# Performance work log

Measured on AMD Instinct MI355X. Metric: run time of the kernel, lower is better.

## Reference

```python
import jax, jax.numpy as jnp
import numpy as np

B, HW, E, H, L, T = 256, 196, 1024, 1024, 128, 48
FC_OUT = L + H + 2  # label | topic | temp | stop


def _linear_params(k, out_d, in_d):
    k1, k2 = jax.random.split(k)
    bound = 1.0 / np.sqrt(in_d)
    W = jax.random.uniform(k1, (out_d, in_d), jnp.float32, -bound, bound)
    b = jax.random.uniform(k2, (out_d,), jnp.float32, -bound, bound)
    return W, b


def setup_inputs() -> dict:
    key = jax.random.key(0)
    ks = jax.random.split(key, 8)
    image = jax.random.normal(ks[0], (B, HW, E), jnp.float32)
    label = jax.random.uniform(ks[1], (B, T, L), jnp.float32)
    # lengths sorted descending (the torch module uses @length_sorted)
    length = jnp.sort(jax.random.randint(ks[2], (B,), 1, T + 1))[::-1]
    W_h, b_h = _linear_params(ks[3], H, E)
    W_m, b_m = _linear_params(ks[4], H, E)
    W_ih, b_ih = _linear_params(ks[5], 4 * H, E + L)
    W_hh, b_hh = _linear_params(ks[6], 4 * H, H)
    W_fc, b_fc = _linear_params(ks[7], FC_OUT, H)
    return {"image": image, "label": label, "length": length,
            "W_h": W_h, "b_h": b_h, "W_m": W_m, "b_m": b_m,
            "W_ih": W_ih, "W_hh": W_hh, "b_ih": b_ih, "b_hh": b_hh,
            "W_fc": W_fc, "b_fc": b_fc}


def reference(image, label, length, W_h, b_h, W_m, b_m, W_ih, W_hh, b_ih, b_hh, W_fc, b_fc):
    # dropout is identity (eval mode)
    img_mean = image.mean(axis=1)                       # (B, E)
    h0 = jnp.tanh(img_mean @ W_h.T + b_h)               # (B, H)
    m0 = jnp.tanh(img_mean @ W_m.T + b_m)               # (B, H)
    lab_t_major = jnp.transpose(label, (1, 0, 2))       # (T, B, L)
    ts = jnp.arange(T)

    def step(carry, inp):
        h, m = carry
        lab_t, t = inp
        x = jnp.concatenate([img_mean, lab_t], axis=-1)          # (B, E+L)
        gates = x @ W_ih.T + b_ih + h @ W_hh.T + b_hh            # (B, 4H), torch order i,f,g,o
        i, f, g, o = jnp.split(gates, 4, axis=-1)
        m = jax.nn.sigmoid(f) * m + jax.nn.sigmoid(i) * jnp.tanh(g)
        h = jax.nn.sigmoid(o) * jnp.tanh(m)
        out = jax.nn.relu(h @ W_fc.T + b_fc)                     # (B, L+H+2)
        _label = out[:, :L]
        _topic = out[:, L:L + H]
        _temp = jnp.exp(out[:, L + H:L + H + 1])
        _stop = jax.nn.sigmoid(out[:, L + H + 1:])
        mask = (t < length)[:, None].astype(out.dtype)           # pad_sequence zero-padding
        return (h, m), (_label * mask, _topic * mask, _temp * mask, _stop * mask)

    _, (lab_o, top_o, temp_o, stop_o) = jax.lax.scan(step, (h0, m0), (lab_t_major, ts))
    # scan stacks on time axis -> (T, B, D); return batch-major (B, T, D)
    return tuple(jnp.transpose(a, (1, 0, 2)) for a in (lab_o, top_o, temp_o, stop_o))
```

## Files before the change

kernel.cpp:

```cpp
#include <hip/hip_runtime.h>

typedef float f32x4 __attribute__((ext_vector_type(4)));
typedef short s16x8 __attribute__((ext_vector_type(8)));
typedef unsigned short u16;

#define B_    256
#define HW_   196
#define E_    1024
#define H_    1024
#define L_    128
#define T_    48
#define FCOUT 1154
#define FCPAD 1216

#define GJOBS 128
#define FJOBS 76

__device__ __forceinline__ u16 f2bf(float x) {
  union { float f; unsigned u; } v; v.f = x;
  unsigned r = v.u + 0x7FFF + ((v.u >> 16) & 1);
  return (u16)(r >> 16);
}
__device__ __forceinline__ float sigm(float x) { return 1.f / (1.f + expf(-x)); }

__global__ __launch_bounds__(256) void cvt_bf16_v4(
    const float* __restrict__ in, u16* __restrict__ out,
    int src_rows, int in_ld, int in_off, int cols4, long total4) {
  long idx = (long)blockIdx.x * 256 + threadIdx.x;
  if (idx >= total4) return;
  int r  = (int)(idx / cols4);
  int c4 = (int)(idx % cols4) * 4;
  f32x4 v = {0.f, 0.f, 0.f, 0.f};
  if (r < src_rows) v = *(const f32x4*)&in[(size_t)r * in_ld + in_off + c4];
  ushort4 o;
  ((u16*)&o)[0] = f2bf(v[0]); ((u16*)&o)[1] = f2bf(v[1]);
  ((u16*)&o)[2] = f2bf(v[2]); ((u16*)&o)[3] = f2bf(v[3]);
  *(ushort4*)&out[idx * 4] = o;
}

__global__ __launch_bounds__(256) void img_mean_k(
    const float* __restrict__ image, u16* __restrict__ meanB) {
  int idx = blockIdx.x * 256 + threadIdx.x;
  int b  = idx >> 8;
  int e4 = (idx & 255) * 4;
  const float* p = image + (size_t)b * HW_ * E_ + e4;
  f32x4 s = {0.f, 0.f, 0.f, 0.f};
  #pragma unroll 4
  for (int hw = 0; hw < HW_; ++hw) s += *(const f32x4*)&p[(size_t)hw * E_];
  ushort4 o;
  #pragma unroll
  for (int c = 0; c < 4; ++c) ((u16*)&o)[c] = f2bf(s[c] * (1.0f / HW_));
  *(ushort4*)&meanB[(size_t)b * E_ + e4] = o;
}

template <int MODE>
__global__ __launch_bounds__(256) void gemm_nt(
    const u16* __restrict__ A, int lda, const u16* __restrict__ Bp, int ldb, int K,
    const float* __restrict__ bias1, const float* __restrict__ bias2,
    float* __restrict__ outF, u16* __restrict__ outB, int ldc) {
  __shared__ __align__(16) u16 As[64][72];
  __shared__ __align__(16) u16 Bs[64][72];

  const int m0 = blockIdx.x * 64;
  const int n0 = blockIdx.y * 64;
  const int tid  = threadIdx.x;
  const int lane = tid & 63;
  const int wave = tid >> 6;
  const int wm = wave & 1, wn = wave >> 1;
  const int quad = lane >> 4, l16 = lane & 15;
  const int loadRow = tid >> 3;
  const int loadCol = (tid & 7) * 8;

  f32x4 acc[2][2] = {};

  for (int kb = 0; kb < K; kb += 64) {
    __syncthreads();
    #pragma unroll
    for (int p = 0; p < 2; ++p) {
      int r = loadRow + p * 32;
      *(uint4*)&As[r][loadCol] = *(const uint4*)&A [(size_t)(m0 + r) * lda + kb + loadCol];
      *(uint4*)&Bs[r][loadCol] = *(const uint4*)&Bp[(size_t)(n0 + r) * ldb + kb + loadCol];
    }
    __syncthreads();
    #pragma unroll
    for (int ks = 0; ks < 64; ks += 32) {
      s16x8 a0v = *(const s16x8*)&As[wm * 32      + l16][ks + quad * 8];
      s16x8 a1v = *(const s16x8*)&As[wm * 32 + 16 + l16][ks + quad * 8];
      s16x8 b0v = *(const s16x8*)&Bs[wn * 32      + l16][ks + quad * 8];
      s16x8 b1v = *(const s16x8*)&Bs[wn * 32 + 16 + l16][ks + quad * 8];
      acc[0][0] = __builtin_amdgcn_mfma_f32_16x16x32_bf16(a0v, b0v, acc[0][0], 0, 0, 0);
      acc[0][1] = __builtin_amdgcn_mfma_f32_16x16x32_bf16(a0v, b1v, acc[0][1], 0, 0, 0);
      acc[1][0] = __builtin_amdgcn_mfma_f32_16x16x32_bf16(a1v, b0v, acc[1][0], 0, 0, 0);
      acc[1][1] = __builtin_amdgcn_mfma_f32_16x16x32_bf16(a1v, b1v, acc[1][1], 0, 0, 0);
    }
  }

  #pragma unroll
  for (int mi = 0; mi < 2; ++mi) {
    #pragma unroll
    for (int ni = 0; ni < 2; ++ni) {
      #pragma unroll
      for (int r = 0; r < 4; ++r) {
        int m = m0 + wm * 32 + mi * 16 + quad * 4 + r;
        int n = n0 + wn * 32 + ni * 16 + l16;
        float v = acc[mi][ni][r];
        if constexpr (MODE == 0) {
          outF[(size_t)m * ldc + n] = v + bias1[n] + bias2[n];
        } else if constexpr (MODE == 1) {
          outB[(size_t)m * ldc + n] = f2bf(tanhf(v + bias1[n]));
        } else {
          outF[(size_t)m * ldc + n] = tanhf(v + bias1[n]);
        }
      }
    }
  }
}

struct GS8 { u16 A[2][32][72]; u16 B[2][256][72]; };
struct FS8 { u16 A[2][64][72]; u16 B[2][64][72]; };
union __align__(16) SharedU {
  GS8 g;
  FS8 f;
  float gs[2][4][32][68];
  float fs[64][68];
};

__global__ __launch_bounds__(512) void step_k(
    const u16* __restrict__ labB,
    const u16* __restrict__ WihL,
    const u16* __restrict__ WhhB,
    const u16* __restrict__ WfcB,
    const float* __restrict__ gbase,
    const float* __restrict__ b_fc,
    const u16* __restrict__ hcur, u16* __restrict__ hnext,
    float* __restrict__ mS,
    const int* __restrict__ length,
    float* __restrict__ out,
    int p) {
  __shared__ SharedU sh;

  const int bid  = blockIdx.x;
  const int tid  = threadIdx.x;
  const int g2   = tid >> 8;
  const int gtid = tid & 255;
  const int lane = tid & 63;
  const int wave = tid >> 6;
  const int sw   = wave & 3;
  const int quad = lane >> 4, l16 = lane & 15;
  const int ar = gtid >> 3;
  const int ac = (gtid & 7) * 8;

  if (p < T_ && bid < GJOBS) {
    const int mb = bid >> 4;
    const int jb = bid & 15;
    f32x4 acc[2][4] = {};

    for (int kb = 0; kb < 9; ++kb) {
      const int seg1 = (g2 == 1) || (kb >= 2);
      const int k0 = g2 ? (448 + kb * 64) : (seg1 ? (kb - 2) * 64 : kb * 64);

      __syncthreads();
      {
        const u16* Ap = seg1
            ? hcur + (size_t)(mb * 32 + ar) * H_ + k0 + ac
            : labB + (size_t)(mb * 32 + ar) * (T_ * L_) + (size_t)p * L_ + k0 + ac;
        *(uint4*)&sh.g.A[g2][ar][ac] = *(const uint4*)Ap;
        const u16* Bw  = seg1 ? WhhB : WihL;
        const int  ldb = seg1 ? H_ : L_;
        #pragma unroll
        for (int q = 0; q < 8; ++q) {
          int rr = ar + q * 32;
          int grow = (rr >> 6) * H_ + jb * 64 + (rr & 63);
          *(uint4*)&sh.g.B[g2][rr][ac] =
              *(const uint4*)&Bw[(size_t)grow * ldb + k0 + ac];
        }
      }
      __syncthreads();
      #pragma unroll
      for (int ks = 0; ks < 64; ks += 32) {
        s16x8 av[2], bv[4];
        av[0] = *(const s16x8*)&sh.g.A[g2][l16][ks + quad * 8];
        av[1] = *(const s16x8*)&sh.g.A[g2][16 + l16][ks + quad * 8];
        #pragma unroll
        for (int ni = 0; ni < 4; ++ni)
          bv[ni] = *(const s16x8*)&sh.g.B[g2][sw * 64 + ni * 16 + l16][ks + quad * 8];
        #pragma unroll
        for (int mi = 0; mi < 2; ++mi)
          #pragma unroll
          for (int ni = 0; ni < 4; ++ni)
            acc[mi][ni] = __builtin_amdgcn_mfma_f32_16x16x32_bf16(
                av[mi], bv[ni], acc[mi][ni], 0, 0, 0);
      }
    }

    __syncthreads();
    #pragma unroll
    for (int mi = 0; mi < 2; ++mi)
      #pragma unroll
      for (int ni = 0; ni < 4; ++ni)
        #pragma unroll
        for (int r = 0; r < 4; ++r)
          sh.gs[g2][sw][mi * 16 + quad * 4 + r][ni * 16 + l16] = acc[mi][ni][r];
    __syncthreads();

    {
      const int bl = tid >> 4, j4 = (tid & 15) * 4;
      const int b = mb * 32 + bl, j = jb * 64 + j4;
      const float* gb = gbase + (size_t)b * (4 * H_) + j;
      f32x4 gi = *(const f32x4*)&sh.gs[0][0][bl][j4] + *(const f32x4*)&sh.gs[1][0][bl][j4];
      f32x4 gf = *(const f32x4*)&sh.gs[0][1][bl][j4] + *(const f32x4*)&sh.gs[1][1][bl][j4];
      f32x4 gg = *(const f32x4*)&sh.gs[0][2][bl][j4] + *(const f32x4*)&sh.gs[1][2][bl][j4];
      f32x4 go = *(const f32x4*)&sh.gs[0][3][bl][j4] + *(const f32x4*)&sh.gs[1][3][bl][j4];
      f32x4 bi  = *(const f32x4*)(gb);
      f32x4 bff = *(const f32x4*)(gb + H_);
      f32x4 bg  = *(const f32x4*)(gb + 2 * H_);
      f32x4 bo  = *(const f32x4*)(gb + 3 * H_);
      float* mp = mS + (size_t)b * H_ + j;
      f32x4 m = *(f32x4*)mp;
      ushort4 hb;
      #pragma unroll
      for (int c = 0; c < 4; ++c) {
        float I = sigm(gi[c] + bi[c]);
        float F = sigm(gf[c] + bff[c]);
        float G = tanhf(gg[c] + bg[c]);
        float O = sigm(go[c] + bo[c]);
        float mm = F * m[c] + I * G;
        m[c] = mm;
        ((u16*)&hb)[c] = f2bf(O * tanhf(mm));
      }
      *(f32x4*)mp = m;
      *(ushort4*)&hnext[(size_t)b * H_ + j] = hb;
    }
  } else if (p >= 1 && bid >= GJOBS && bid < GJOBS + FJOBS) {
    const int t   = p - 1;
    const int fid = bid - GJOBS;
    const int m0 = (fid / 19) * 64;
    const int n0 = (fid % 19) * 64;
    const int wm = sw & 1, wn = sw >> 1;
    f32x4 acc[2][2] = {};

    for (int kb = 0; kb < 8; ++kb) {
      const int k0 = g2 * 512 + kb * 64;
      __syncthreads();
      #pragma unroll
      for (int pp = 0; pp < 2; ++pp) {
        int r = ar + pp * 32;
        *(uint4*)&sh.f.A[g2][r][ac] = *(const uint4*)&hcur[(size_t)(m0 + r) * H_ + k0 + ac];
        *(uint4*)&sh.f.B[g2][r][ac] = *(const uint4*)&WfcB[(size_t)(n0 + r) * H_ + k0 + ac];
      }
      __syncthreads();
      #pragma unroll
      for (int ks = 0; ks < 64; ks += 32) {
        s16x8 a0v = *(const s16x8*)&sh.f.A[g2][wm * 32      + l16][ks + quad * 8];
        s16x8 a1v = *(const s16x8*)&sh.f.A[g2][wm * 32 + 16 + l16][ks + quad * 8];
        s16x8 b0v = *(const s16x8*)&sh.f.B[g2][wn * 32      + l16][ks + quad * 8];
        s16x8 b1v = *(const s16x8*)&sh.f.B[g2][wn * 32 + 16 + l16][ks + quad * 8];
        acc[0][0] = __builtin_amdgcn_mfma_f32_16x16x32_bf16(a0v, b0v, acc[0][0], 0, 0, 0);
        acc[0][1] = __builtin_amdgcn_mfma_f32_16x16x32_bf16(a0v, b1v, acc[0][1], 0, 0, 0);
        acc[1][0] = __builtin_amdgcn_mfma_f32_16x16x32_bf16(a1v, b0v, acc[1][0], 0, 0, 0);
        acc[1][1] = __builtin_amdgcn_mfma_f32_16x16x32_bf16(a1v, b1v, acc[1][1], 0, 0, 0);
      }
    }

    __syncthreads();
    if (g2 == 1) {
      #pragma unroll
      for (int mi = 0; mi < 2; ++mi)
        #pragma unroll
        for (int ni = 0; ni < 2; ++ni)
          #pragma unroll
          for (int r = 0; r < 4; ++r)
            sh.fs[wm * 32 + mi * 16 + quad * 4 + r][wn * 32 + ni * 16 + l16] =
                acc[mi][ni][r];
    }
    __syncthreads();
    if (g2 == 0) {
      #pragma unroll
      for (int mi = 0; mi < 2; ++mi) {
        #pragma unroll
        for (int ni = 0; ni < 2; ++ni) {
          #pragma unroll
          for (int r = 0; r < 4; ++r) {
            int ml = wm * 32 + mi * 16 + quad * 4 + r;
            int nl = wn * 32 + ni * 16 + l16;
            int m = m0 + ml;
            int n = n0 + nl;
            if (n < FCOUT) {
              float rv = fmaxf(acc[mi][ni][r] + sh.fs[ml][nl] + b_fc[n], 0.f);
              float msk = (t < length[m]) ? 1.f : 0.f;
              if (n < L_) {
                out[(size_t)m * (T_ * L_) + t * L_ + n] = rv * msk;
              } else if (n < L_ + H_) {
                out[(size_t)(B_ * T_ * L_) + (size_t)m * (T_ * H_) + t * H_ + (n - L_)] = rv * msk;
              } else if (n == L_ + H_) {
                out[(size_t)B_ * T_ * (L_ + H_) + m * T_ + t] = expf(rv) * msk;
              } else {
                out[(size_t)B_ * T_ * (L_ + H_ + 1) + m * T_ + t] = sigm(rv) * msk;
              }
            }
          }
        }
      }
    }
  }
}

extern "C" void kernel_launch(void* const* d_in, const int* in_sizes, int n_in,
                              void* d_out, int out_size, void* d_ws, size_t ws_size,
                              hipStream_t stream) {
  const float* image  = (const float*)d_in[0];
  const float* label  = (const float*)d_in[1];
  const int*   length = (const int*)  d_in[2];
  const float* W_h    = (const float*)d_in[3];
  const float* b_h    = (const float*)d_in[4];
  const float* W_m    = (const float*)d_in[5];
  const float* b_m    = (const float*)d_in[6];
  const float* W_ih   = (const float*)d_in[7];
  const float* W_hh   = (const float*)d_in[8];
  const float* b_ih   = (const float*)d_in[9];
  const float* b_hh   = (const float*)d_in[10];
  const float* W_fc   = (const float*)d_in[11];
  const float* b_fc   = (const float*)d_in[12];
  float* out = (float*)d_out;

  char* ws = (char*)d_ws;
  size_t off = 0;
  auto alloc = [&](size_t bytes) -> void* {
    void* p = ws + off;
    off = (off + bytes + 255) & ~(size_t)255;
    return p;
  };
  u16*   meanB = (u16*)  alloc((size_t)B_ * E_ * 2);
  u16*   WhB   = (u16*)  alloc((size_t)H_ * E_ * 2);
  u16*   WmB   = (u16*)  alloc((size_t)H_ * E_ * 2);
  u16*   WihE  = (u16*)  alloc((size_t)4 * H_ * E_ * 2);
  u16*   WihL  = (u16*)  alloc((size_t)4 * H_ * L_ * 2);
  u16*   WhhB  = (u16*)  alloc((size_t)4 * H_ * H_ * 2);
  u16*   WfcB  = (u16*)  alloc((size_t)FCPAD * H_ * 2);
  u16*   labB  = (u16*)  alloc((size_t)B_ * T_ * L_ * 2);
  float* gbase = (float*)alloc((size_t)B_ * 4 * H_ * 4);
  u16*   hbuf0 = (u16*)  alloc((size_t)B_ * H_ * 2);
  u16*   hbuf1 = (u16*)  alloc((size_t)B_ * H_ * 2);
  float* mS    = (float*)alloc((size_t)B_ * H_ * 4);

  auto cvt = [&](const float* in, u16* o, int rows, int src_rows, int in_ld,
                 int in_off, int cols) {
    long total4 = (long)rows * cols / 4;
    int blocks = (int)((total4 + 255) / 256);
    cvt_bf16_v4<<<blocks, 256, 0, stream>>>(in, o, src_rows, in_ld, in_off,
                                            cols / 4, total4);
  };

  cvt(W_h,  WhB,  H_,     H_,     E_,      0,  E_);
  cvt(W_m,  WmB,  H_,     H_,     E_,      0,  E_);
  cvt(W_ih, WihE, 4 * H_, 4 * H_, E_ + L_, 0,  E_);
  cvt(W_ih, WihL, 4 * H_, 4 * H_, E_ + L_, E_, L_);
  cvt(W_hh, WhhB, 4 * H_, 4 * H_, H_,      0,  H_);
  cvt(W_fc, WfcB, FCPAD,  FCOUT,  H_,      0,  H_);
  cvt(label, labB, B_, B_, T_ * L_, 0, T_ * L_);

  img_mean_k<<<(B_ * E_ / 4) / 256, 256, 0, stream>>>(image, meanB);

  gemm_nt<1><<<dim3(B_ / 64, H_ / 64), 256, 0, stream>>>(
      meanB, E_, WhB, E_, E_, b_h, nullptr, nullptr, hbuf0, H_);
  gemm_nt<2><<<dim3(B_ / 64, H_ / 64), 256, 0, stream>>>(
      meanB, E_, WmB, E_, E_, b_m, nullptr, mS, nullptr, H_);
  gemm_nt<0><<<dim3(B_ / 64, (4 * H_) / 64), 256, 0, stream>>>(
      meanB, E_, WihE, E_, E_, b_ih, b_hh, gbase, nullptr, 4 * H_);

  for (int p = 0; p <= T_; ++p) {
    u16* hcur  = (p & 1) ? hbuf1 : hbuf0;
    u16* hnext = (p & 1) ? hbuf0 : hbuf1;
    step_k<<<GJOBS + FJOBS, 512, 0, stream>>>(
        labB, WihL, WhhB, WfcB, gbase, b_fc, hcur, hnext, mS, length, out, p);
  }
}
```

Measured before the change: 1.298 ms.

## Enlarge LSTM gate tiles to 64 rows and remap block-to-tile assignment

Each gate block now covers 64 batch rows instead of 32, so the gate GEMM uses 64 blocks instead of 128. Each block reuses its loaded W_hh/W_ih tile across twice as many rows, roughly halving weight traffic per step. The two K-halves are reduced through shared memory in two phases instead of being kept as separate buffers. FC blocks are remapped onto 96 slots (76 active) with an ordering that appears to group work for cache locality. The trade-off is fewer blocks, which lowers parallelism and occupancy, and higher register pressure from the 4x4 accumulator array.

```diff
diff --git a/kernel.cpp b/kernel.cpp
--- a/kernel.cpp
+++ b/kernel.cpp
@@ -13,8 +13,9 @@
 #define FCOUT 1154
 #define FCPAD 1216
 
-#define GJOBS 128
-#define FJOBS 76
+#define GB_    64
+#define FBASE_ 64
+#define FSLOT_ 96
 
 __device__ __forceinline__ u16 f2bf(float x) {
   union { float f; unsigned u; } v; v.f = x;
@@ -116,12 +117,12 @@
   }
 }
 
-struct GS8 { u16 A[2][32][72]; u16 B[2][256][72]; };
-struct FS8 { u16 A[2][64][72]; u16 B[2][64][72]; };
+struct GS { u16 A[2][64][72]; u16 B[2][256][72]; };
+struct FS { u16 A[2][64][72]; u16 B[2][64][72]; };
 union __align__(16) SharedU {
-  GS8 g;
-  FS8 f;
-  float gs[2][4][32][68];
+  GS g;
+  FS f;
+  float ex[4][64][68];
   float fs[64][68];
 };
 
@@ -150,10 +151,11 @@
   const int ar = gtid >> 3;
   const int ac = (gtid & 7) * 8;
 
-  if (p < T_ && bid < GJOBS) {
-    const int mb = bid >> 4;
-    const int jb = bid & 15;
-    f32x4 acc[2][4] = {};
+  if (p < T_ && bid < GB_) {
+    const int q8 = bid >> 3;
+    const int mb = q8 & 3;
+    const int jb = (bid & 7) + 8 * (q8 >> 2);
+    f32x4 acc[4][4] = {};
 
     for (int kb = 0; kb < 9; ++kb) {
       const int seg1 = (g2 == 1) || (kb >= 2);
@@ -161,15 +163,19 @@
 
       __syncthreads();
       {
-        const u16* Ap = seg1
-            ? hcur + (size_t)(mb * 32 + ar) * H_ + k0 + ac
-            : labB + (size_t)(mb * 32 + ar) * (T_ * L_) + (size_t)p * L_ + k0 + ac;
-        *(uint4*)&sh.g.A[g2][ar][ac] = *(const uint4*)Ap;
+        #pragma unroll
+        for (int pp = 0; pp < 2; ++pp) {
+          int r = ar + pp * 32;
+          const u16* Ap = seg1
+              ? hcur + (size_t)(mb * 64 + r) * H_ + k0 + ac
+              : labB + (size_t)(mb * 64 + r) * (T_ * L_) + (size_t)p * L_ + k0 + ac;
+          *(uint4*)&sh.g.A[g2][r][ac] = *(const uint4*)Ap;
+        }
         const u16* Bw  = seg1 ? WhhB : WihL;
         const int  ldb = seg1 ? H_ : L_;
         #pragma unroll
-        for (int q = 0; q < 8; ++q) {
-          int rr = ar + q * 32;
+        for (int qq = 0; qq < 8; ++qq) {
+          int rr = ar + qq * 32;
           int grow = (rr >> 6) * H_ + jb * 64 + (rr & 63);
           *(uint4*)&sh.g.B[g2][rr][ac] =
               *(const uint4*)&Bw[(size_t)grow * ldb + k0 + ac];
@@ -178,14 +184,15 @@
       __syncthreads();
       #pragma unroll
       for (int ks = 0; ks < 64; ks += 32) {
-        s16x8 av[2], bv[4];
-        av[0] = *(const s16x8*)&sh.g.A[g2][l16][ks + quad * 8];
-        av[1] = *(const s16x8*)&sh.g.A[g2][16 + l16][ks + quad * 8];
+        s16x8 av[4], bv[4];
+        #pragma unroll
+        for (int mi = 0; mi < 4; ++mi)
+          av[mi] = *(const s16x8*)&sh.g.A[g2][mi * 16 + l16][ks + quad * 8];
         #pragma unroll
         for (int ni = 0; ni < 4; ++ni)
           bv[ni] = *(const s16x8*)&sh.g.B[g2][sw * 64 + ni * 16 + l16][ks + quad * 8];
         #pragma unroll
-        for (int mi = 0; mi < 2; ++mi)
+        for (int mi = 0; mi < 4; ++mi)
           #pragma unroll
           for (int ni = 0; ni < 4; ++ni)
             acc[mi][ni] = __builtin_amdgcn_mfma_f32_16x16x32_bf16(
@@ -194,48 +201,68 @@
     }
 
     __syncthreads();
-    #pragma unroll
-    for (int mi = 0; mi < 2; ++mi)
-      #pragma unroll
-      for (int ni = 0; ni < 4; ++ni)
-        #pragma unroll
-        for (int r = 0; r < 4; ++r)
-          sh.gs[g2][sw][mi * 16 + quad * 4 + r][ni * 16 + l16] = acc[mi][ni][r];
+    if (g2 == 1) {
+      #pragma unroll
+      for (int mi = 0; mi < 4; ++mi)
+        #pragma unroll
+        for (int ni = 0; ni < 4; ++ni)
+          #pragma unroll
+          for (int r = 0; r < 4; ++r)
+            sh.ex[sw][mi * 16 + quad * 4 + r][ni * 16 + l16] = acc[mi][ni][r];
+    }
+    __syncthreads();
+    if (g2 == 0) {
+      #pragma unroll
+      for (int mi = 0; mi < 4; ++mi)
+        #pragma unroll
+        for (int ni = 0; ni < 4; ++ni)
+          #pragma unroll
+          for (int r = 0; r < 4; ++r)
+            sh.ex[sw][mi * 16 + quad * 4 + r][ni * 16 + l16] += acc[mi][ni][r];
+    }
     __syncthreads();
 
     {
-      const int bl = tid >> 4, j4 = (tid & 15) * 4;
-      const int b = mb * 32 + bl, j = jb * 64 + j4;
+      const int bl = tid >> 3, j8 = (tid & 7) * 8;
+      const int b = mb * 64 + bl, j = jb * 64 + j8;
       const float* gb = gbase + (size_t)b * (4 * H_) + j;
-      f32x4 gi = *(const f32x4*)&sh.gs[0][0][bl][j4] + *(const f32x4*)&sh.gs[1][0][bl][j4];
-      f32x4 gf = *(const f32x4*)&sh.gs[0][1][bl][j4] + *(const f32x4*)&sh.gs[1][1][bl][j4];
-      f32x4 gg = *(const f32x4*)&sh.gs[0][2][bl][j4] + *(const f32x4*)&sh.gs[1][2][bl][j4];
-      f32x4 go = *(const f32x4*)&sh.gs[0][3][bl][j4] + *(const f32x4*)&sh.gs[1][3][bl][j4];
-      f32x4 bi  = *(const f32x4*)(gb);
-      f32x4 bff = *(const f32x4*)(gb + H_);
-      f32x4 bg  = *(const f32x4*)(gb + 2 * H_);
-      f32x4 bo  = *(const f32x4*)(gb + 3 * H_);
       float* mp = mS + (size_t)b * H_ + j;
-      f32x4 m = *(f32x4*)mp;
-      ushort4 hb;
-      #pragma unroll
-      for (int c = 0; c < 4; ++c) {
-        float I = sigm(gi[c] + bi[c]);
-        float F = sigm(gf[c] + bff[c]);
-        float G = tanhf(gg[c] + bg[c]);
-        float O = sigm(go[c] + bo[c]);
-        float mm = F * m[c] + I * G;
-        m[c] = mm;
-        ((u16*)&hb)[c] = f2bf(O * tanhf(mm));
-      }
-      *(f32x4*)mp = m;
-      *(ushort4*)&hnext[(size_t)b * H_ + j] = hb;
-    }
-  } else if (p >= 1 && bid >= GJOBS && bid < GJOBS + FJOBS) {
-    const int t   = p - 1;
-    const int fid = bid - GJOBS;
-    const int m0 = (fid / 19) * 64;
-    const int n0 = (fid % 19) * 64;
+      u16 hb[8];
+      #pragma unroll
+      for (int h4 = 0; h4 < 2; ++h4) {
+        const int jl = j8 + h4 * 4;
+        f32x4 gi = *(const f32x4*)&sh.ex[0][bl][jl];
+        f32x4 gf = *(const f32x4*)&sh.ex[1][bl][jl];
+        f32x4 gg = *(const f32x4*)&sh.ex[2][bl][jl];
+        f32x4 go = *(const f32x4*)&sh.ex[3][bl][jl];
+        f32x4 bi  = *(const f32x4*)(gb + h4 * 4);
+        f32x4 bff = *(const f32x4*)(gb + H_ + h4 * 4);
+        f32x4 bg  = *(const f32x4*)(gb + 2 * H_ + h4 * 4);
+        f32x4 bo  = *(const f32x4*)(gb + 3 * H_ + h4 * 4);
+        f32x4 m = *(f32x4*)(mp + h4 * 4);
+        #pragma unroll
+        for (int c = 0; c < 4; ++c) {
+          float I = sigm(gi[c] + bi[c]);
+          float F = sigm(gf[c] + bff[c]);
+          float G = tanhf(gg[c] + bg[c]);
+          float O = sigm(go[c] + bo[c]);
+          float mm = F * m[c] + I * G;
+          m[c] = mm;
+          hb[h4 * 4 + c] = f2bf(O * tanhf(mm));
+        }
+        *(f32x4*)(mp + h4 * 4) = m;
+      }
+      *(uint4*)&hnext[(size_t)b * H_ + j] = *(const uint4*)hb;
+    }
+  } else if (p >= 1 && bid >= FBASE_ && bid < FBASE_ + FSLOT_) {
+    const int t    = p - 1;
+    const int fidx = bid - FBASE_;
+    const int rres = fidx & 7, kk = fidx >> 3;
+    const int fm = kk & 3, nhi = kk >> 2;
+    const int fn = rres + 8 * nhi;
+    if (fn >= 19) return;
+    const int m0 = fm * 64;
+    const int n0 = fn * 64;
     const int wm = sw & 1, wn = sw >> 1;
     f32x4 acc[2][2] = {};
 
@@ -371,7 +398,7 @@
   for (int p = 0; p <= T_; ++p) {
     u16* hcur  = (p & 1) ? hbuf1 : hbuf0;
     u16* hnext = (p & 1) ? hbuf0 : hbuf1;
-    step_k<<<GJOBS + FJOBS, 512, 0, stream>>>(
+    step_k<<<FBASE_ + FSLOT_, 512, 0, stream>>>(
         labB, WihL, WhhB, WfcB, gbase, b_fc, hcur, hnext, mS, length, out, p);
   }
 }
```

Result: slower. 1.571 ms (+21.0%).

## Fuse per-timestep launches into one persistent kernel with grid barrier

Applied to the files above, without the earlier changes.

Replaces the 49 per-timestep step_k launches with a single persistent scan_k kernel that loops over timesteps and synchronizes all 204 blocks through an atomic counter and generation grid barrier. The cell state and gate bias tile now stay in registers and LDS across steps instead of round-tripping through global memory. Blocks whose batch rows have already ended skip the gate and FC math and write zeros directly, using the descending sorted lengths. h is read and written with agent-scope atomics so it is visible across blocks. The risk is the cost of the software barrier, and a deadlock if the 204 blocks are not all resident at once.

```diff
diff --git a/kernel.cpp b/kernel.cpp
--- a/kernel.cpp
+++ b/kernel.cpp
@@ -15,6 +15,7 @@
 
 #define GJOBS 128
 #define FJOBS 76
+#define NBLK  (GJOBS + FJOBS)
 
 __device__ __forceinline__ u16 f2bf(float x) {
   union { float f; unsigned u; } v; v.f = x;
@@ -22,6 +23,33 @@
   return (u16)(r >> 16);
 }
 __device__ __forceinline__ float sigm(float x) { return 1.f / (1.f + expf(-x)); }
+
+__device__ __forceinline__ uint2 ld_h8(const u16* p) {
+  unsigned long long v = __hip_atomic_load((const unsigned long long*)p,
+                                           __ATOMIC_RELAXED, __HIP_MEMORY_SCOPE_AGENT);
+  union { unsigned long long u; uint2 d; } c; c.u = v; return c.d;
+}
+__device__ __forceinline__ void st_h8(u16* p, ushort4 s) {
+  union { ushort4 s; unsigned long long u; } c; c.s = s;
+  __hip_atomic_store((unsigned long long*)p, c.u,
+                     __ATOMIC_RELAXED, __HIP_MEMORY_SCOPE_AGENT);
+}
+
+__device__ __forceinline__ void gbar(int* cnt, int* gen) {
+  __syncthreads();
+  if (threadIdx.x == 0) {
+    int g = __hip_atomic_load(gen, __ATOMIC_RELAXED, __HIP_MEMORY_SCOPE_AGENT);
+    int a = __hip_atomic_fetch_add(cnt, 1, __ATOMIC_ACQ_REL, __HIP_MEMORY_SCOPE_AGENT);
+    if (a == NBLK - 1) {
+      __hip_atomic_store(cnt, 0, __ATOMIC_RELAXED, __HIP_MEMORY_SCOPE_AGENT);
+      __hip_atomic_store(gen, g + 1, __ATOMIC_RELEASE, __HIP_MEMORY_SCOPE_AGENT);
+    } else {
+      while (__hip_atomic_load(gen, __ATOMIC_ACQUIRE, __HIP_MEMORY_SCOPE_AGENT) == g)
+        __builtin_amdgcn_s_sleep(2);
+    }
+  }
+  __syncthreads();
+}
 
 __global__ __launch_bounds__(256) void cvt_bf16_v4(
     const float* __restrict__ in, u16* __restrict__ out,
@@ -125,19 +153,20 @@
   float fs[64][68];
 };
 
-__global__ __launch_bounds__(512) void step_k(
+__global__ __launch_bounds__(512) void scan_k(
     const u16* __restrict__ labB,
     const u16* __restrict__ WihL,
     const u16* __restrict__ WhhB,
     const u16* __restrict__ WfcB,
     const float* __restrict__ gbase,
     const float* __restrict__ b_fc,
-    const u16* __restrict__ hcur, u16* __restrict__ hnext,
-    float* __restrict__ mS,
+    u16* __restrict__ hb0, u16* __restrict__ hb1,
+    const float* __restrict__ mS0,
     const int* __restrict__ length,
     float* __restrict__ out,
-    int p) {
+    int* __restrict__ barCnt, int* __restrict__ barGen) {
   __shared__ SharedU sh;
+  __shared__ __align__(16) float gbs[4][32][64];
 
   const int bid  = blockIdx.x;
   const int tid  = threadIdx.x;
@@ -150,158 +179,196 @@
   const int ar = gtid >> 3;
   const int ac = (gtid & 7) * 8;
 
-  if (p < T_ && bid < GJOBS) {
-    const int mb = bid >> 4;
-    const int jb = bid & 15;
-    f32x4 acc[2][4] = {};
-
-    for (int kb = 0; kb < 9; ++kb) {
-      const int seg1 = (g2 == 1) || (kb >= 2);
-      const int k0 = g2 ? (448 + kb * 64) : (seg1 ? (kb - 2) * 64 : kb * 64);
-
-      __syncthreads();
-      {
-        const u16* Ap = seg1
-            ? hcur + (size_t)(mb * 32 + ar) * H_ + k0 + ac
-            : labB + (size_t)(mb * 32 + ar) * (T_ * L_) + (size_t)p * L_ + k0 + ac;
-        *(uint4*)&sh.g.A[g2][ar][ac] = *(const uint4*)Ap;
-        const u16* Bw  = seg1 ? WhhB : WihL;
-        const int  ldb = seg1 ? H_ : L_;
-        #pragma unroll
-        for (int q = 0; q < 8; ++q) {
-          int rr = ar + q * 32;
-          int grow = (rr >> 6) * H_ + jb * 64 + (rr & 63);
-          *(uint4*)&sh.g.B[g2][rr][ac] =
-              *(const uint4*)&Bw[(size_t)grow * ldb + k0 + ac];
-        }
-      }
-      __syncthreads();
-      #pragma unroll
-      for (int ks = 0; ks < 64; ks += 32) {
-        s16x8 av[2], bv[4];
-        av[0] = *(const s16x8*)&sh.g.A[g2][l16][ks + quad * 8];
-        av[1] = *(const s16x8*)&sh.g.A[g2][16 + l16][ks + quad * 8];
-        #pragma unroll
-        for (int ni = 0; ni < 4; ++ni)
-          bv[ni] = *(const s16x8*)&sh.g.B[g2][sw * 64 + ni * 16 + l16][ks + quad * 8];
+  const bool isG = bid < GJOBS;
+  int mb = 0, jb = 0, m0 = 0, n0 = 0, glen = 0;
+  f32x4 mreg = {0.f, 0.f, 0.f, 0.f};
+
+  if (isG) {
+    jb = (bid & 7) * 2 + ((bid >> 3) & 1);
+    mb = bid >> 4;
+    glen = length[mb * 32];
+    const int bl = tid >> 4, j4 = (tid & 15) * 4;
+    #pragma unroll
+    for (int g = 0; g < 4; ++g)
+      *(f32x4*)&gbs[g][bl][j4] =
+          *(const f32x4*)&gbase[(size_t)(mb * 32 + bl) * (4 * H_) + g * H_ + jb * 64 + j4];
+    mreg = *(const f32x4*)&mS0[(size_t)(mb * 32 + bl) * H_ + jb * 64 + j4];
+  } else {
+    const int fid = bid - GJOBS;
+    m0 = (fid / 19) * 64;
+    n0 = (fid % 19) * 64;
+    glen = length[m0];
+  }
+
+  for (int p = 0; p <= T_; ++p) {
+    u16* hcur  = (p & 1) ? hb1 : hb0;
+    u16* hnext = (p & 1) ? hb0 : hb1;
+
+    if (isG) {
+      if (p < T_ && glen > p) {
+        f32x4 acc[2][4] = {};
+        for (int kb = 0; kb < 9; ++kb) {
+          const int seg1 = (g2 == 1) || (kb >= 2);
+          const int k0 = g2 ? (448 + kb * 64) : (seg1 ? (kb - 2) * 64 : kb * 64);
+          __syncthreads();
+          if (seg1) {
+            const u16* Ap = hcur + (size_t)(mb * 32 + ar) * H_ + k0 + ac;
+            *(uint2*)&sh.g.A[g2][ar][ac]     = ld_h8(Ap);
+            *(uint2*)&sh.g.A[g2][ar][ac + 4] = ld_h8(Ap + 4);
+          } else {
+            *(uint4*)&sh.g.A[g2][ar][ac] = *(const uint4*)
+                &labB[(size_t)(mb * 32 + ar) * (T_ * L_) + (size_t)p * L_ + k0 + ac];
+          }
+          const u16* Bw  = seg1 ? WhhB : WihL;
+          const int  ldb = seg1 ? H_ : L_;
+          #pragma unroll
+          for (int q = 0; q < 8; ++q) {
+            int rr = ar + q * 32;
+            int grow = (rr >> 6) * H_ + jb * 64 + (rr & 63);
+            *(uint4*)&sh.g.B[g2][rr][ac] =
+                *(const uint4*)&Bw[(size_t)grow * ldb + k0 + ac];
+          }
+          __syncthreads();
+          #pragma unroll
+          for (int ks = 0; ks < 64; ks += 32) {
+            s16x8 av[2], bv[4];
+            av[0] = *(const s16x8*)&sh.g.A[g2][l16][ks + quad * 8];
+            av[1] = *(const s16x8*)&sh.g.A[g2][16 + l16][ks + quad * 8];
+            #pragma unroll
+            for (int ni = 0; ni < 4; ++ni)
+              bv[ni] = *(const s16x8*)&sh.g.B[g2][sw * 64 + ni * 16 + l16][ks + quad * 8];
+            #pragma unroll
+            for (int mi = 0; mi < 2; ++mi)
+              #pragma unroll
+              for (int ni = 0; ni < 4; ++ni)
+                acc[mi][ni] = __builtin_amdgcn_mfma_f32_16x16x32_bf16(
+                    av[mi], bv[ni], acc[mi][ni], 0, 0, 0);
+          }
+        }
+
+        __syncthreads();
         #pragma unroll
         for (int mi = 0; mi < 2; ++mi)
           #pragma unroll
           for (int ni = 0; ni < 4; ++ni)
-            acc[mi][ni] = __builtin_amdgcn_mfma_f32_16x16x32_bf16(
-                av[mi], bv[ni], acc[mi][ni], 0, 0, 0);
+            #pragma unroll
+            for (int r = 0; r < 4; ++r)
+              sh.gs[g2][sw][mi * 16 + quad * 4 + r][ni * 16 + l16] = acc[mi][ni][r];
+        __syncthreads();
+
+        {
+          const int bl = tid >> 4, j4 = (tid & 15) * 4;
+          f32x4 gi = *(const f32x4*)&sh.gs[0][0][bl][j4] + *(const f32x4*)&sh.gs[1][0][bl][j4];
+          f32x4 gf = *(const f32x4*)&sh.gs[0][1][bl][j4] + *(const f32x4*)&sh.gs[1][1][bl][j4];
+          f32x4 gg = *(const f32x4*)&sh.gs[0][2][bl][j4] + *(const f32x4*)&sh.gs[1][2][bl][j4];
+          f32x4 go = *(const f32x4*)&sh.gs[0][3][bl][j4] + *(const f32x4*)&sh.gs[1][3][bl][j4];
+          f32x4 bi  = *(const f32x4*)&gbs[0][bl][j4];
+          f32x4 bff = *(const f32x4*)&gbs[1][bl][j4];
+          f32x4 bg  = *(const f32x4*)&gbs[2][bl][j4];
+          f32x4 bo  = *(const f32x4*)&gbs[3][bl][j4];
+          ushort4 hb;
+          #pragma unroll
+          for (int c = 0; c < 4; ++c) {
+            float I = sigm(gi[c] + bi[c]);
+            float F = sigm(gf[c] + bff[c]);
+            float G = tanhf(gg[c] + bg[c]);
+            float O = sigm(go[c] + bo[c]);
+            float mm = F * mreg[c] + I * G;
+            mreg[c] = mm;
+            ((u16*)&hb)[c] = f2bf(O * tanhf(mm));
+          }
+          st_h8(&hnext[(size_t)(mb * 32 + bl) * H_ + jb * 64 + j4], hb);
+        }
+      }
+    } else if (p >= 1) {
+      const int t = p - 1;
+      if (glen > t) {
+        const int wm = sw & 1, wn = sw >> 1;
+        f32x4 acc[2][2] = {};
+        for (int kb = 0; kb < 8; ++kb) {
+          const int k0 = g2 * 512 + kb * 64;
+          __syncthreads();
+          #pragma unroll
+          for (int pp = 0; pp < 2; ++pp) {
+            int r = ar + pp * 32;
+            const u16* Ap = hcur + (size_t)(m0 + r) * H_ + k0 + ac;
+            *(uint2*)&sh.f.A[g2][r][ac]     = ld_h8(Ap);
+            *(uint2*)&sh.f.A[g2][r][ac + 4] = ld_h8(Ap + 4);
+            *(uint4*)&sh.f.B[g2][r][ac] =
+                *(const uint4*)&WfcB[(size_t)(n0 + r) * H_ + k0 + ac];
+          }
+          __syncthreads();
+          #pragma unroll
+          for (int ks = 0; ks < 64; ks += 32) {
+            s16x8 a0v = *(const s16x8*)&sh.f.A[g2][wm * 32      + l16][ks + quad * 8];
+            s16x8 a1v = *(const s16x8*)&sh.f.A[g2][wm * 32 + 16 + l16][ks + quad * 8];
+            s16x8 b0v = *(const s16x8*)&sh.f.B[g2][wn * 32      + l16][ks + quad * 8];
+            s16x8 b1v = *(const s16x8*)&sh.f.B[g2][wn * 32 + 16 + l16][ks + quad * 8];
+            acc[0][0] = __builtin_amdgcn_mfma_f32_16x16x32_bf16(a0v, b0v, acc[0][0], 0, 0, 0);
+            acc[0][1] = __builtin_amdgcn_mfma_f32_16x16x32_bf16(a0v, b1v, acc[0][1], 0, 0, 0);
+            acc[1][0] = __builtin_amdgcn_mfma_f32_16x16x32_bf16(a1v, b0v, acc[1][0], 0, 0, 0);
+            acc[1][1] = __builtin_amdgcn_mfma_f32_16x16x32_bf16(a1v, b1v, acc[1][1], 0, 0, 0);
+          }
+        }
+
+        __syncthreads();
+        if (g2 == 1) {
+          #pragma unroll
+          for (int mi = 0; mi < 2; ++mi)
+            #pragma unroll
+            for (int ni = 0; ni < 2; ++ni)
+              #pragma unroll
+              for (int r = 0; r < 4; ++r)
+                sh.fs[wm * 32 + mi * 16 + quad * 4 + r][wn * 32 + ni * 16 + l16] =
+                    acc[mi][ni][r];
+        }
+        __syncthreads();
+        if (g2 == 0) {
+          #pragma unroll
+          for (int mi = 0; mi < 2; ++mi) {
+            #pragma unroll
+            for (int ni = 0; ni < 2; ++ni) {
+              #pragma unroll
+              for (int r = 0; r < 4; ++r) {
+                int ml = wm * 32 + mi * 16 + quad * 4 + r;
+                int nl = wn * 32 + ni * 16 + l16;
+                int m = m0 + ml;
+                int n = n0 + nl;
+                if (n < FCOUT) {
+                  float rv = fmaxf(acc[mi][ni][r] + sh.fs[ml][nl] + b_fc[n], 0.f);
+                  float msk = (t < length[m]) ? 1.f : 0.f;
+                  if (n < L_) {
+                    out[(size_t)m * (T_ * L_) + t * L_ + n] = rv * msk;
+                  } else if (n < L_ + H_) {
+                    out[(size_t)(B_ * T_ * L_) + (size_t)m * (T_ * H_) + t * H_ + (n - L_)] = rv * msk;
+                  } else if (n == L_ + H_) {
+                    out[(size_t)B_ * T_ * (L_ + H_) + m * T_ + t] = expf(rv) * msk;
+                  } else {
+                    out[(size_t)B_ * T_ * (L_ + H_ + 1) + m * T_ + t] = sigm(rv) * msk;
+                  }
+                }
+              }
+            }
+          }
+        }
+      } else if (n0 == 0) {
+        f32x4 z = {0.f, 0.f, 0.f, 0.f};
+        for (int i = tid; i < 64 * 32; i += 512) {
+          int r = i >> 5, c4 = (i & 31) * 4;
+          *(f32x4*)&out[(size_t)(m0 + r) * (T_ * L_) + t * L_ + c4] = z;
+        }
+        for (int i = tid; i < 64 * 256; i += 512) {
+          int r = i >> 8, c4 = (i & 255) * 4;
+          *(f32x4*)&out[(size_t)(B_ * T_ * L_) + (size_t)(m0 + r) * (T_ * H_) + t * H_ + c4] = z;
+        }
+        if (tid < 64) {
+          out[(size_t)B_ * T_ * (L_ + H_) + (m0 + tid) * T_ + t] = 0.f;
+          out[(size_t)B_ * T_ * (L_ + H_ + 1) + (m0 + tid) * T_ + t] = 0.f;
+        }
       }
     }
 
-    __syncthreads();
-    #pragma unroll
-    for (int mi = 0; mi < 2; ++mi)
-      #pragma unroll
-      for (int ni = 0; ni < 4; ++ni)
-        #pragma unroll
-        for (int r = 0; r < 4; ++r)
-          sh.gs[g2][sw][mi * 16 + quad * 4 + r][ni * 16 + l16] = acc[mi][ni][r];
-    __syncthreads();
-
-    {
-      const int bl = tid >> 4, j4 = (tid & 15) * 4;
-      const int b = mb * 32 + bl, j = jb * 64 + j4;
-      const float* gb = gbase + (size_t)b * (4 * H_) + j;
-      f32x4 gi = *(const f32x4*)&sh.gs[0][0][bl][j4] + *(const f32x4*)&sh.gs[1][0][bl][j4];
-      f32x4 gf = *(const f32x4*)&sh.gs[0][1][bl][j4] + *(const f32x4*)&sh.gs[1][1][bl][j4];
-      f32x4 gg = *(const f32x4*)&sh.gs[0][2][bl][j4] + *(const f32x4*)&sh.gs[1][2][bl][j4];
-      f32x4 go = *(const f32x4*)&sh.gs[0][3][bl][j4] + *(const f32x4*)&sh.gs[1][3][bl][j4];
-      f32x4 bi  = *(const f32x4*)(gb);
-      f32x4 bff = *(const f32x4*)(gb + H_);
-      f32x4 bg  = *(const f32x4*)(gb + 2 * H_);
-      f32x4 bo  = *(const f32x4*)(gb + 3 * H_);
-      float* mp = mS + (size_t)b * H_ + j;
-      f32x4 m = *(f32x4*)mp;
-      ushort4 hb;
-      #pragma unroll
-      for (int c = 0; c < 4; ++c) {
-        float I = sigm(gi[c] + bi[c]);
-        float F = sigm(gf[c] + bff[c]);
-        float G = tanhf(gg[c] + bg[c]);
-        float O = sigm(go[c] + bo[c]);
-        float mm = F * m[c] + I * G;
-        m[c] = mm;
-        ((u16*)&hb)[c] = f2bf(O * tanhf(mm));
-      }
-      *(f32x4*)mp = m;
-      *(ushort4*)&hnext[(size_t)b * H_ + j] = hb;
-    }
-  } else if (p >= 1 && bid >= GJOBS && bid < GJOBS + FJOBS) {
-    const int t   = p - 1;
-    const int fid = bid - GJOBS;
-    const int m0 = (fid / 19) * 64;
-    const int n0 = (fid % 19) * 64;
-    const int wm = sw & 1, wn = sw >> 1;
-    f32x4 acc[2][2] = {};
-
-    for (int kb = 0; kb < 8; ++kb) {
-      const int k0 = g2 * 512 + kb * 64;
-      __syncthreads();
-      #pragma unroll
-      for (int pp = 0; pp < 2; ++pp) {
-        int r = ar + pp * 32;
-        *(uint4*)&sh.f.A[g2][r][ac] = *(const uint4*)&hcur[(size_t)(m0 + r) * H_ + k0 + ac];
-        *(uint4*)&sh.f.B[g2][r][ac] = *(const uint4*)&WfcB[(size_t)(n0 + r) * H_ + k0 + ac];
-      }
-      __syncthreads();
-      #pragma unroll
-      for (int ks = 0; ks < 64; ks += 32) {
-        s16x8 a0v = *(const s16x8*)&sh.f.A[g2][wm * 32      + l16][ks + quad * 8];
-        s16x8 a1v = *(const s16x8*)&sh.f.A[g2][wm * 32 + 16 + l16][ks + quad * 8];
-        s16x8 b0v = *(const s16x8*)&sh.f.B[g2][wn * 32      + l16][ks + quad * 8];
-        s16x8 b1v = *(const s16x8*)&sh.f.B[g2][wn * 32 + 16 + l16][ks + quad * 8];
-        acc[0][0] = __builtin_amdgcn_mfma_f32_16x16x32_bf16(a0v, b0v, acc[0][0], 0, 0, 0);
-        acc[0][1] = __builtin_amdgcn_mfma_f32_16x16x32_bf16(a0v, b1v, acc[0][1], 0, 0, 0);
-        acc[1][0] = __builtin_amdgcn_mfma_f32_16x16x32_bf16(a1v, b0v, acc[1][0], 0, 0, 0);
-        acc[1][1] = __builtin_amdgcn_mfma_f32_16x16x32_bf16(a1v, b1v, acc[1][1], 0, 0, 0);
-      }
-    }
-
-    __syncthreads();
-    if (g2 == 1) {
-      #pragma unroll
-      for (int mi = 0; mi < 2; ++mi)
-        #pragma unroll
-        for (int ni = 0; ni < 2; ++ni)
-          #pragma unroll
-          for (int r = 0; r < 4; ++r)
-            sh.fs[wm * 32 + mi * 16 + quad * 4 + r][wn * 32 + ni * 16 + l16] =
-                acc[mi][ni][r];
-    }
-    __syncthreads();
-    if (g2 == 0) {
-      #pragma unroll
-      for (int mi = 0; mi < 2; ++mi) {
-        #pragma unroll
-        for (int ni = 0; ni < 2; ++ni) {
-          #pragma unroll
-          for (int r = 0; r < 4; ++r) {
-            int ml = wm * 32 + mi * 16 + quad * 4 + r;
-            int nl = wn * 32 + ni * 16 + l16;
-            int m = m0 + ml;
-            int n = n0 + nl;
-            if (n < FCOUT) {
-              float rv = fmaxf(acc[mi][ni][r] + sh.fs[ml][nl] + b_fc[n], 0.f);
-              float msk = (t < length[m]) ? 1.f : 0.f;
-              if (n < L_) {
-                out[(size_t)m * (T_ * L_) + t * L_ + n] = rv * msk;
-              } else if (n < L_ + H_) {
-                out[(size_t)(B_ * T_ * L_) + (size_t)m * (T_ * H_) + t * H_ + (n - L_)] = rv * msk;
-              } else if (n == L_ + H_) {
-                out[(size_t)B_ * T_ * (L_ + H_) + m * T_ + t] = expf(rv) * msk;
-              } else {
-                out[(size_t)B_ * T_ * (L_ + H_ + 1) + m * T_ + t] = sigm(rv) * msk;
-              }
-            }
-          }
-        }
-      }
-    }
+    gbar(barCnt, barGen);
   }
 }
 
@@ -342,6 +409,7 @@
   u16*   hbuf0 = (u16*)  alloc((size_t)B_ * H_ * 2);
   u16*   hbuf1 = (u16*)  alloc((size_t)B_ * H_ * 2);
   float* mS    = (float*)alloc((size_t)B_ * H_ * 4);
+  int*   bar   = (int*)  alloc(256);
 
   auto cvt = [&](const float* in, u16* o, int rows, int src_rows, int in_ld,
                  int in_off, int cols) {
@@ -368,10 +436,8 @@
   gemm_nt<0><<<dim3(B_ / 64, (4 * H_) / 64), 256, 0, stream>>>(
       meanB, E_, WihE, E_, E_, b_ih, b_hh, gbase, nullptr, 4 * H_);
 
-  for (int p = 0; p <= T_; ++p) {
-    u16* hcur  = (p & 1) ? hbuf1 : hbuf0;
-    u16* hnext = (p & 1) ? hbuf0 : hbuf1;
-    step_k<<<GJOBS + FJOBS, 512, 0, stream>>>(
-        labB, WihL, WhhB, WfcB, gbase, b_fc, hcur, hnext, mS, length, out, p);
-  }
-}
+  hipMemsetAsync(bar, 0, 8, stream);
+  scan_k<<<NBLK, 512, 0, stream>>>(
+      labB, WihL, WhhB, WfcB, gbase, b_fc, hbuf0, hbuf1, mS, length, out,
+      bar, bar + 1);
+}
```

Measured after the change: 3.125 ms. 141% more time.
